# Kernel tuning notes

Hardware: AMD Instinct MI355X
Metric: run time of the kernel (lower is better)

Reference implementation:

```python
import jax, jax.numpy as jnp
import numpy as np

D_MODEL = 1024
HEADS = 16
D_K = D_MODEL // HEADS
B, S = 2, 2048


def setup_inputs() -> dict:
    key = jax.random.key(0)
    ks = jax.random.split(key, 11)
    sc = 1.0 / np.sqrt(D_MODEL)
    return {
        "q": jax.random.normal(ks[0], (B, S, D_MODEL), jnp.float32),
        "k": jax.random.normal(ks[1], (B, S, D_MODEL), jnp.float32),
        "v": jax.random.normal(ks[2], (B, S, D_MODEL), jnp.float32),
        "Wq": jax.random.normal(ks[3], (D_MODEL, D_MODEL), jnp.float32) * sc,
        "bq": jnp.zeros((D_MODEL,), jnp.float32),
        "Wk": jax.random.normal(ks[4], (D_MODEL, D_MODEL), jnp.float32) * sc,
        "bk": jnp.zeros((D_MODEL,), jnp.float32),
        "Wv": jax.random.normal(ks[5], (D_MODEL, D_MODEL), jnp.float32) * sc,
        "bv": jnp.zeros((D_MODEL,), jnp.float32),
        "Wo": jax.random.normal(ks[6], (D_MODEL, D_MODEL), jnp.float32) * sc,
        "bo": jnp.zeros((D_MODEL,), jnp.float32),
    }


def reference(q, k, v, Wq, bq, Wk, bk, Wv, bv, Wo, bo):
    bs = q.shape[0]
    # linear projections then split heads: [B,S,D] -> [B,H,S,Dk]
    def proj(x, W, b):
        y = x @ W.T + b
        return y.reshape(bs, -1, HEADS, D_K).transpose(0, 2, 1, 3)

    qh = proj(q, Wq, bq)
    kh = proj(k, Wk, bk)
    vh = proj(v, Wv, bv)
    # scores: [B,H,Sq,Sk] -- full attention matrix as in the original
    scores = jnp.einsum("bhqd,bhkd->bhqk", qh, kh) / jnp.sqrt(
        jnp.asarray(D_K, jnp.float32))
    attn = jax.nn.softmax(scores, axis=-1)
    # dropout is identity in eval/reference mode
    out = jnp.einsum("bhqk,bhkd->bhqd", attn, vh)
    concat = out.transpose(0, 2, 1, 3).reshape(bs, -1, D_MODEL)
    return concat @ Wo.T + bo
```

## Files before the change

kernel.cpp:

```cpp
#include <hip/hip_runtime.h>
#include <hip/hip_bf16.h>

typedef __attribute__((ext_vector_type(8))) short bf16x8;
typedef __attribute__((ext_vector_type(4))) float f32x4;
typedef __attribute__((ext_vector_type(16))) float f32x16;

#define DM   1024
#define SEQ  2048
#define NB   2
#define NH   16
#define MR   (NB*SEQ)

#define SMK  (MR*DM)
#define W1M  (DM*DM)

#define QSCALE 0.18033688011112042f

#define OFF_QB  ((size_t)0)
#define OFF_KB  ((size_t)SMK)
#define OFF_VB  ((size_t)(2*(size_t)SMK))
#define OFF_WQ  ((size_t)(3*(size_t)SMK))
#define OFF_WO  ((size_t)(3*(size_t)SMK + 3*(size_t)W1M))
#define OFF_QP  ((size_t)(3*(size_t)SMK + 4*(size_t)W1M))
#define OFF_KP  ((size_t)(4*(size_t)SMK + 4*(size_t)W1M))
#define OFF_VP  ((size_t)(5*(size_t)SMK + 4*(size_t)W1M))
#define OFF_CC  ((size_t)0)

__device__ __forceinline__ unsigned short f2bf(float f) {
  union { __hip_bfloat16 b; unsigned short u; } cv;
  cv.b = __float2bfloat16(f);
  return cv.u;
}

__device__ __forceinline__ unsigned int cvtpk_bf16(float lo, float hi) {
  unsigned int r;
  asm("v_cvt_pk_bf16_f32 %0, %1, %2" : "=v"(r) : "v"(lo), "v"(hi));
  return r;
}

__device__ __forceinline__ void plane32_swap(unsigned int& a, unsigned int& b) {
  asm("v_permlane32_swap_b32 %0, %1" : "+v"(a), "+v"(b));
}

__global__ __launch_bounds__(256) void cvt_inputs(const float* __restrict__ q,
                                                  const float* __restrict__ k,
                                                  const float* __restrict__ v,
                                                  unsigned short* __restrict__ dst) {
  const int z = blockIdx.y;
  const float* src = (z == 0) ? q : ((z == 1) ? k : v);
  int i = blockIdx.x * 256 + threadIdx.x;
  float4 val = reinterpret_cast<const float4*>(src)[i];
  ushort4 o;
  o.x = f2bf(val.x); o.y = f2bf(val.y); o.z = f2bf(val.z); o.w = f2bf(val.w);
  reinterpret_cast<ushort4*>(dst + (size_t)z * SMK)[i] = o;
}

__global__ __launch_bounds__(256) void cvt_weights(const float* __restrict__ wq,
                                                   const float* __restrict__ wk,
                                                   const float* __restrict__ wv,
                                                   const float* __restrict__ wo,
                                                   unsigned short* __restrict__ dst) {
  const int z = blockIdx.y;
  const float* src = (z == 0) ? wq : ((z == 1) ? wk : ((z == 2) ? wv : wo));
  int i = blockIdx.x * 256 + threadIdx.x;
  float4 val = reinterpret_cast<const float4*>(src)[i];
  ushort4 o;
  o.x = f2bf(val.x); o.y = f2bf(val.y); o.z = f2bf(val.z); o.w = f2bf(val.w);
  reinterpret_cast<ushort4*>(dst + (size_t)z * W1M)[i] = o;
}

__device__ __forceinline__ void gload_lds16(const void* g, void* l) {
  __builtin_amdgcn_global_load_lds(
      (const __attribute__((address_space(1))) unsigned int*)g,
      (__attribute__((address_space(3))) unsigned int*)l,
      16, 0, 0);
}

template<int BM, int BN, bool OUT_BF16, bool BIAS_ROW>
__device__ __forceinline__ void gemm_bt_body(unsigned short* __restrict__ As,
                                             unsigned short* __restrict__ Bs,
                                             const unsigned short* __restrict__ A,
                                             const unsigned short* __restrict__ Bt,
                                             const float* __restrict__ bias,
                                             void* __restrict__ Cv,
                                             int N, int K, float scale,
                                             int brow, int bcol) {
  constexpr int MREP = BM / 32;
  constexpr int NREP = BN / 32;
  const int tid  = threadIdx.x;
  const int lane = tid & 63;
  const int w    = tid >> 6;
  const int wr   = w >> 1, wc = w & 1;

  f32x4 acc[MREP][NREP];
#pragma unroll
  for (int m = 0; m < MREP; m++)
#pragma unroll
    for (int n = 0; n < NREP; n++) acc[m][n] = (f32x4){0.f, 0.f, 0.f, 0.f};

  const int srow = lane >> 2;
  const int scol = (lane & 3) * 8;

  auto stage = [&](int buf, int k0) {
#pragma unroll
    for (int c = w; c < BM / 16; c += 4)
      gload_lds16(A + (size_t)(brow + c * 16 + srow) * K + k0 + scol,
                  (char*)As + (size_t)buf * BM * 64 + c * 1024);
#pragma unroll
    for (int c = w; c < BN / 16; c += 4)
      gload_lds16(Bt + (size_t)(bcol + c * 16 + srow) * K + k0 + scol,
                  (char*)Bs + (size_t)buf * BN * 64 + c * 1024);
  };

  stage(0, 0);
  __syncthreads();

  const int nk = K / 32;
  const int lrow_a = wr * (BM / 2) + (lane & 15);
  const int lrow_b = wc * (BN / 2) + (lane & 15);
  const int lcol   = (lane >> 4) * 8;

  for (int kt = 0; kt < nk; ++kt) {
    int buf = kt & 1;
    if (kt + 1 < nk) stage(buf ^ 1, (kt + 1) * 32);
    bf16x8 a[MREP], b[NREP];
#pragma unroll
    for (int m = 0; m < MREP; m++)
      a[m] = *(const bf16x8*)&As[(size_t)buf * BM * 32 + (lrow_a + m * 16) * 32 + lcol];
#pragma unroll
    for (int n = 0; n < NREP; n++)
      b[n] = *(const bf16x8*)&Bs[(size_t)buf * BN * 32 + (lrow_b + n * 16) * 32 + lcol];
    __builtin_amdgcn_s_setprio(1);
#pragma unroll
    for (int m = 0; m < MREP; m++)
#pragma unroll
      for (int n = 0; n < NREP; n++)
        acc[m][n] = __builtin_amdgcn_mfma_f32_16x16x32_bf16(a[m], b[n], acc[m][n], 0, 0, 0);
    __builtin_amdgcn_s_setprio(0);
    __syncthreads();
  }

  const int crow0 = brow + wr * (BM / 2);
  const int ccol0 = bcol + wc * (BN / 2);
  const int rsub  = (lane >> 4) * 4;
  const int csub  = lane & 15;
#pragma unroll
  for (int m = 0; m < MREP; m++)
#pragma unroll
    for (int n = 0; n < NREP; n++) {
      int col = ccol0 + n * 16 + csub;
      float bcol_v = BIAS_ROW ? 0.f : bias[col];
#pragma unroll
      for (int q = 0; q < 4; q++) {
        int row = crow0 + m * 16 + rsub + q;
        float bb = BIAS_ROW ? bias[row] : bcol_v;
        float v = (acc[m][n][q] + bb) * scale;
        if (OUT_BF16)
          ((unsigned short*)Cv)[(size_t)row * N + col] = f2bf(v);
        else
          ((float*)Cv)[(size_t)row * N + col] = v;
      }
    }
}

__global__ __launch_bounds__(256) void gemm_qkv(unsigned short* ws,
                                                const float* __restrict__ bq,
                                                const float* __restrict__ bk,
                                                const float* __restrict__ bv) {
  __shared__ unsigned short As[2 * 128 * 32];
  __shared__ unsigned short Bs[2 * 128 * 32];
  const int z = blockIdx.z;
  const int bid = blockIdx.x;
  if (z < 2) {
    int bx = bid & 7, by = bid >> 3;
    gemm_bt_body<128, 128, true, false>(
        As, Bs,
        ws + OFF_QB + (size_t)z * SMK, ws + OFF_WQ + (size_t)z * W1M,
        z ? bk : bq, ws + OFF_QP + (size_t)z * SMK,
        DM, DM, z ? 1.f : QSCALE, by * 128, bx * 128);
  } else {
    int bx = bid & 31, by = bid >> 5;
    gemm_bt_body<128, 128, true, true>(
        As, Bs,
        ws + OFF_WQ + 2 * W1M, ws + OFF_VB,
        bv, ws + OFF_VP,
        MR, DM, 1.f, by * 128, bx * 128);
  }
}

__global__ __launch_bounds__(256) void gemm_out(const unsigned short* __restrict__ ws,
                                                const float* __restrict__ bo,
                                                float* __restrict__ out) {
  __shared__ unsigned short As[2 * 64 * 32];
  __shared__ unsigned short Bs[2 * 128 * 32];
  gemm_bt_body<64, 128, false, false>(
      As, Bs,
      ws + OFF_CC, ws + OFF_WO, bo, out,
      DM, DM, 1.f, blockIdx.y * 64, blockIdx.x * 128);
}

__global__ __launch_bounds__(256) void flash_attn(unsigned short* ws) {
  __shared__ unsigned short Ks[2][64 * 64];
  __shared__ unsigned short Vs[2][64 * 64];

  const int tid  = threadIdx.x;
  const int lane = tid & 63;
  const int w    = tid >> 6;
  const int q    = lane & 31;
  const int hi   = lane >> 5;
  const int swq  = q & 7;
  const int bid  = blockIdx.x;
  const int swzb = (bid & 7) * 64 + (bid >> 3);
  const int qblk = swzb & 15;
  const int bh   = swzb >> 4;
  const int b    = bh >> 4, h = bh & 15;

  const unsigned short* Qp = ws + OFF_QP;
  const unsigned short* Kp = ws + OFF_KP;
  const unsigned short* Vp = ws + OFF_VP;
  unsigned short* CC = ws + OFF_CC;

  const unsigned short* Kg = Kp + (size_t)(b * SEQ) * DM + h * 64;
  const unsigned short* Vg = Vp + (size_t)(h * 64) * MR + (size_t)b * SEQ;

  bf16x8 bqf[4];
  {
    const unsigned short* qrow =
        Qp + (size_t)(b * SEQ + qblk * 128 + w * 32 + q) * DM + h * 64;
#pragma unroll
    for (int c = 0; c < 4; c++)
      bqf[c] = *(const bf16x8*)(qrow + c * 16 + hi * 8);
  }

  f32x16 o_acc[2];
#pragma unroll
  for (int dt = 0; dt < 2; dt++)
#pragma unroll
    for (int r = 0; r < 16; r++) o_acc[dt][r] = 0.f;
  float l_run = 0.f;

  auto stage = [&](unsigned short* lds, const unsigned short* gbase, int stride) {
#pragma unroll
    for (int sh = 0; sh < 2; sh++) {
      int slot = sh * 256 + w * 64 + lane;
      int srow = slot >> 3;
      int gch  = (slot & 7) ^ (srow & 7);
      gload_lds16(gbase + (size_t)srow * stride + gch * 8,
                  (char*)lds + (size_t)(sh * 256 + w * 64) * 16);
    }
  };

  stage(Ks[0], Kg, DM);
  stage(Vs[0], Vg, MR);

  for (int kt = 0; kt < SEQ / 64; ++kt) {
    int buf = kt & 1;
    __syncthreads();
    if (kt + 1 < SEQ / 64) {
      stage(Ks[buf ^ 1], Kg + (size_t)(kt + 1) * 64 * DM, DM);
      stage(Vs[buf ^ 1], Vg + (kt + 1) * 64, MR);
    }
    const unsigned short* Kb = Ks[buf];
    const unsigned short* Vb = Vs[buf];

    f32x16 st0, st1;
#pragma unroll
    for (int r = 0; r < 16; r++) { st0[r] = 0.f; st1[r] = 0.f; }
    __builtin_amdgcn_s_setprio(1);
#pragma unroll
    for (int c = 0; c < 4; c++) {
      int ch = (((c << 1) | hi) ^ swq) << 3;
      bf16x8 ak0 = *(const bf16x8*)&Kb[q * 64 + ch];
      bf16x8 ak1 = *(const bf16x8*)&Kb[(32 + q) * 64 + ch];
      st0 = __builtin_amdgcn_mfma_f32_32x32x16_bf16(ak0, bqf[c], st0, 0, 0, 0);
      st1 = __builtin_amdgcn_mfma_f32_32x32x16_bf16(ak1, bqf[c], st1, 0, 0, 0);
    }
    __builtin_amdgcn_s_setprio(0);

    unsigned int pk0[8], pk1[8];
    float lt = 0.f;
#pragma unroll
    for (int p = 0; p < 8; p++) {
      float a0 = __builtin_amdgcn_exp2f(st0[2 * p]);
      float a1 = __builtin_amdgcn_exp2f(st0[2 * p + 1]);
      float b0 = __builtin_amdgcn_exp2f(st1[2 * p]);
      float b1 = __builtin_amdgcn_exp2f(st1[2 * p + 1]);
      lt += (a0 + a1) + (b0 + b1);
      pk0[p] = cvtpk_bf16(a0, a1);
      pk1[p] = cvtpk_bf16(b0, b1);
    }
    l_run += lt;

    plane32_swap(pk0[0], pk0[2]); plane32_swap(pk0[1], pk0[3]);
    plane32_swap(pk0[4], pk0[6]); plane32_swap(pk0[5], pk0[7]);
    plane32_swap(pk1[0], pk1[2]); plane32_swap(pk1[1], pk1[3]);
    plane32_swap(pk1[4], pk1[6]); plane32_swap(pk1[5], pk1[7]);

    __builtin_amdgcn_s_setprio(1);
#pragma unroll
    for (int t = 0; t < 4; t++) {
      union { unsigned int u[4]; bf16x8 v; } pb;
      const unsigned int* src = (t < 2) ? pk0 : pk1;
      pb.u[0] = src[(t & 1) * 4 + 0];
      pb.u[1] = src[(t & 1) * 4 + 1];
      pb.u[2] = src[(t & 1) * 4 + 2];
      pb.u[3] = src[(t & 1) * 4 + 3];
      int ch = (((t << 1) | hi) ^ swq) << 3;
#pragma unroll
      for (int dt = 0; dt < 2; dt++) {
        bf16x8 av = *(const bf16x8*)&Vb[(dt * 32 + q) * 64 + ch];
        o_acc[dt] = __builtin_amdgcn_mfma_f32_32x32x16_bf16(av, pb.v, o_acc[dt], 0, 0, 0);
      }
    }
    __builtin_amdgcn_s_setprio(0);
  }

  float l = l_run + __shfl_xor(l_run, 32, 64);
  float inv = 1.f / l;
  int qg = b * SEQ + qblk * 128 + w * 32 + q;
  unsigned short* crow = CC + (size_t)qg * DM + h * 64;
#pragma unroll
  for (int dt = 0; dt < 2; dt++)
#pragma unroll
    for (int rq = 0; rq < 4; rq++) {
      ushort4 o;
      o.x = f2bf(o_acc[dt][4 * rq + 0] * inv);
      o.y = f2bf(o_acc[dt][4 * rq + 1] * inv);
      o.z = f2bf(o_acc[dt][4 * rq + 2] * inv);
      o.w = f2bf(o_acc[dt][4 * rq + 3] * inv);
      *(ushort4*)&crow[dt * 32 + rq * 8 + hi * 4] = o;
    }
}

extern "C" void kernel_launch(void* const* d_in, const int* in_sizes, int n_in,
                              void* d_out, int out_size, void* d_ws, size_t ws_size,
                              hipStream_t stream) {
  const float* q  = (const float*)d_in[0];
  const float* k  = (const float*)d_in[1];
  const float* v  = (const float*)d_in[2];
  const float* Wq = (const float*)d_in[3];
  const float* bq = (const float*)d_in[4];
  const float* Wk = (const float*)d_in[5];
  const float* bk = (const float*)d_in[6];
  const float* Wv = (const float*)d_in[7];
  const float* bv = (const float*)d_in[8];
  const float* Wo = (const float*)d_in[9];
  const float* bo = (const float*)d_in[10];

  unsigned short* ws = (unsigned short*)d_ws;
  float* out = (float*)d_out;

  cvt_inputs<<<dim3(SMK / 1024, 3), dim3(256), 0, stream>>>(q, k, v, ws + OFF_QB);
  cvt_weights<<<dim3(W1M / 1024, 4), dim3(256), 0, stream>>>(Wq, Wk, Wv, Wo, ws + OFF_WQ);

  gemm_qkv<<<dim3(256, 1, 3), dim3(256), 0, stream>>>(ws, bq, bk, bv);

  flash_attn<<<dim3(512), dim3(256), 0, stream>>>(ws);

  gemm_out<<<dim3(DM / 128, MR / 64, 1), dim3(256), 0, stream>>>(ws, bo, out);
}
```

Baseline: 132.7 us.

## Split flash attention KV sequence across two wave groups per block with LDS reduction

Flash attention blocks now use 512 threads: two groups of four waves each process half of the key/value sequence for the same 128 query rows, with separate double-buffered LDS tiles per group. At the end the second group writes its partial output accumulators and row sums to shared memory, and the first group adds them, normalizes and stores the result. This doubles the waves per block to raise latency hiding and MFMA utilization with the same 512-block grid. In exchange it adds an LDS reduction step and a 64KB shared-memory footprint that may limit occupancy. No running max is used in either half, so merging the two halves by simple addition stays correct.

Result: faster. 126.0 us (-5.1%).

```diff
diff --git a/kernel.cpp b/kernel.cpp
--- a/kernel.cpp
+++ b/kernel.cpp
@@ -199,13 +199,14 @@
       DM, DM, 1.f, blockIdx.y * 64, blockIdx.x * 128);
 }
 
-__global__ __launch_bounds__(256) void flash_attn(unsigned short* ws) {
-  __shared__ unsigned short Ks[2][64 * 64];
-  __shared__ unsigned short Vs[2][64 * 64];
+__global__ __launch_bounds__(512, 4) void flash_attn(unsigned short* ws) {
+  __shared__ __align__(16) unsigned char smem[65536];
 
   const int tid  = threadIdx.x;
   const int lane = tid & 63;
   const int w    = tid >> 6;
+  const int s    = w >> 2;
+  const int wsub = w & 3;
   const int q    = lane & 31;
   const int hi   = lane >> 5;
   const int swq  = q & 7;
@@ -226,7 +227,7 @@
   bf16x8 bqf[4];
   {
     const unsigned short* qrow =
-        Qp + (size_t)(b * SEQ + qblk * 128 + w * 32 + q) * DM + h * 64;
+        Qp + (size_t)(b * SEQ + qblk * 128 + wsub * 32 + q) * DM + h * 64;
 #pragma unroll
     for (int c = 0; c < 4; c++)
       bqf[c] = *(const bf16x8*)(qrow + c * 16 + hi * 8);
@@ -239,29 +240,28 @@
     for (int r = 0; r < 16; r++) o_acc[dt][r] = 0.f;
   float l_run = 0.f;
 
-  auto stage = [&](unsigned short* lds, const unsigned short* gbase, int stride) {
-#pragma unroll
-    for (int sh = 0; sh < 2; sh++) {
-      int slot = sh * 256 + w * 64 + lane;
+  auto stage = [&](int buf, int t) {
+    const unsigned short* Kt = Kg + (size_t)(s * 16 + t) * 64 * DM;
+    const unsigned short* Vt = Vg + (s * 16 + t) * 64;
+    char* base = (char*)smem + (size_t)(s * 2 + buf) * 16384;
+#pragma unroll
+    for (int i = 0; i < 2; i++) {
+      int slot = wsub * 128 + i * 64 + lane;
       int srow = slot >> 3;
       int gch  = (slot & 7) ^ (srow & 7);
-      gload_lds16(gbase + (size_t)srow * stride + gch * 8,
-                  (char*)lds + (size_t)(sh * 256 + w * 64) * 16);
+      gload_lds16(Kt + (size_t)srow * DM + gch * 8, base + slot * 16);
+      gload_lds16(Vt + (size_t)srow * MR + gch * 8, base + 8192 + slot * 16);
     }
   };
 
-  stage(Ks[0], Kg, DM);
-  stage(Vs[0], Vg, MR);
-
-  for (int kt = 0; kt < SEQ / 64; ++kt) {
-    int buf = kt & 1;
+  stage(0, 0);
+
+  for (int t = 0; t < 16; ++t) {
+    int buf = t & 1;
     __syncthreads();
-    if (kt + 1 < SEQ / 64) {
-      stage(Ks[buf ^ 1], Kg + (size_t)(kt + 1) * 64 * DM, DM);
-      stage(Vs[buf ^ 1], Vg + (kt + 1) * 64, MR);
-    }
-    const unsigned short* Kb = Ks[buf];
-    const unsigned short* Vb = Vs[buf];
+    if (t + 1 < 16) stage(buf ^ 1, t + 1);
+    const unsigned short* Kb = (const unsigned short*)(smem + (size_t)(s * 2 + buf) * 16384);
+    const unsigned short* Vb = Kb + 4096;
 
     f32x16 st0, st1;
 #pragma unroll
@@ -298,14 +298,14 @@
 
     __builtin_amdgcn_s_setprio(1);
 #pragma unroll
-    for (int t = 0; t < 4; t++) {
+    for (int t4 = 0; t4 < 4; t4++) {
       union { unsigned int u[4]; bf16x8 v; } pb;
-      const unsigned int* src = (t < 2) ? pk0 : pk1;
-      pb.u[0] = src[(t & 1) * 4 + 0];
-      pb.u[1] = src[(t & 1) * 4 + 1];
-      pb.u[2] = src[(t & 1) * 4 + 2];
-      pb.u[3] = src[(t & 1) * 4 + 3];
-      int ch = (((t << 1) | hi) ^ swq) << 3;
+      const unsigned int* src = (t4 < 2) ? pk0 : pk1;
+      pb.u[0] = src[(t4 & 1) * 4 + 0];
+      pb.u[1] = src[(t4 & 1) * 4 + 1];
+      pb.u[2] = src[(t4 & 1) * 4 + 2];
+      pb.u[3] = src[(t4 & 1) * 4 + 3];
+      int ch = (((t4 << 1) | hi) ^ swq) << 3;
 #pragma unroll
       for (int dt = 0; dt < 2; dt++) {
         bf16x8 av = *(const bf16x8*)&Vb[(dt * 32 + q) * 64 + ch];
@@ -315,21 +315,41 @@
     __builtin_amdgcn_s_setprio(0);
   }
 
-  float l = l_run + __shfl_xor(l_run, 32, 64);
-  float inv = 1.f / l;
-  int qg = b * SEQ + qblk * 128 + w * 32 + q;
-  unsigned short* crow = CC + (size_t)qg * DM + h * 64;
-#pragma unroll
-  for (int dt = 0; dt < 2; dt++)
-#pragma unroll
-    for (int rq = 0; rq < 4; rq++) {
-      ushort4 o;
-      o.x = f2bf(o_acc[dt][4 * rq + 0] * inv);
-      o.y = f2bf(o_acc[dt][4 * rq + 1] * inv);
-      o.z = f2bf(o_acc[dt][4 * rq + 2] * inv);
-      o.w = f2bf(o_acc[dt][4 * rq + 3] * inv);
-      *(ushort4*)&crow[dt * 32 + rq * 8 + hi * 4] = o;
-    }
+  __syncthreads();
+  float* scr = (float*)smem;
+  float lsum = l_run + __shfl_xor(l_run, 32, 64);
+  if (s == 1) {
+    int idx = (wsub * 64 + lane) * 33;
+#pragma unroll
+    for (int dt = 0; dt < 2; dt++)
+#pragma unroll
+      for (int r = 0; r < 16; r++) scr[idx + dt * 16 + r] = o_acc[dt][r];
+    scr[idx + 32] = lsum;
+  }
+  __syncthreads();
+  if (s == 0) {
+    int idx = (wsub * 64 + lane) * 33;
+#pragma unroll
+    for (int dt = 0; dt < 2; dt++)
+#pragma unroll
+      for (int r = 0; r < 16; r++) o_acc[dt][r] += scr[idx + dt * 16 + r];
+    float l = lsum + scr[idx + 32];
+    float inv = 1.f / l;
+
+    int qg = b * SEQ + qblk * 128 + wsub * 32 + q;
+    unsigned short* crow = CC + (size_t)qg * DM + h * 64;
+#pragma unroll
+    for (int dt = 0; dt < 2; dt++)
+#pragma unroll
+      for (int rq = 0; rq < 4; rq++) {
+        ushort4 o;
+        o.x = f2bf(o_acc[dt][4 * rq + 0] * inv);
+        o.y = f2bf(o_acc[dt][4 * rq + 1] * inv);
+        o.z = f2bf(o_acc[dt][4 * rq + 2] * inv);
+        o.w = f2bf(o_acc[dt][4 * rq + 3] * inv);
+        *(ushort4*)&crow[dt * 32 + rq * 8 + hi * 4] = o;
+      }
+  }
 }
 
 extern "C" void kernel_launch(void* const* d_in, const int* in_sizes, int n_in,
@@ -355,7 +375,7 @@
 
   gemm_qkv<<<dim3(256, 1, 3), dim3(256), 0, stream>>>(ws, bq, bk, bv);
 
-  flash_attn<<<dim3(512), dim3(256), 0, stream>>>(ws);
+  flash_attn<<<dim3(512), dim3(512), 0, stream>>>(ws);
 
   gemm_out<<<dim3(DM / 128, MR / 64, 1), dim3(256), 0, stream>>>(ws, bo, out);
 }
```
